# Optimization experiments

Measured on AMD Instinct MI355X. Metric: run time of the kernel, lower is better.

## Reference

```python
import jax, jax.numpy as jnp
import numpy as np

L, B, S, KV, H, D, HID, FF = 4, 16, 16, 2048, 6, 128, 768, 2048


def apply_rope(x, positions, max_wavelength=10000.0):
    # x: [B, S, H, D], positions: [B, S]; computed in float32 as in the torch code
    d_half = x.shape[-1] // 2
    freq_exponents = (2.0 / x.shape[-1]) * jnp.arange(d_half, dtype=jnp.float32)
    timescale = max_wavelength ** freq_exponents  # [d_half]
    radians = positions[..., None].astype(jnp.float32) / timescale[None, None, :]
    radians = radians[..., None, :]  # [B, S, 1, d_half]
    sin, cos = jnp.sin(radians), jnp.cos(radians)
    xf = x.astype(jnp.float32)
    x1, x2 = xf[..., :d_half], xf[..., d_half:]
    out = jnp.concatenate([x1 * cos - x2 * sin, x2 * cos + x1 * sin], axis=-1)
    return out.astype(x.dtype)


def rms_norm(x, w, eps=1e-6):
    var = jnp.mean(jnp.square(x.astype(jnp.float32)), axis=-1, keepdims=True)
    return (x.astype(jnp.float32) * jax.lax.rsqrt(var + eps)).astype(x.dtype) * w


def make_att_2d_masks(pad_masks, att_masks):
    # cumsum-comparison prefix-LM / block-causal mask (big_vision style)
    cumsum = jnp.cumsum(att_masks, axis=1)
    att_2d = cumsum[:, None, :] <= cumsum[:, :, None]
    pad_2d = pad_masks[:, None, :] & pad_masks[:, :, None]
    return att_2d & pad_2d


def setup_inputs() -> dict:
    key = jax.random.key(0)
    ks = jax.random.split(key, 20)
    sc = 0.02
    inputs_embeds = jax.random.normal(ks[0], (B, S, HID), jnp.float32)
    position_ids = jnp.broadcast_to(KV + jnp.arange(S, dtype=jnp.int64)[None, :], (B, S))
    pad_masks = jnp.ones((B, KV + S), dtype=bool)
    # prefix-LM: prefix tokens bidirectional (0), expert suffix causal (1)
    att_masks = jnp.concatenate([jnp.zeros((B, KV), jnp.int32), jnp.ones((B, S), jnp.int32)], axis=1)
    k_cache = jax.random.normal(ks[1], (L, B, H, KV, D), jnp.float32)
    v_cache = jax.random.normal(ks[2], (L, B, H, KV, D), jnp.float32)
    p = {
        'Wq': jax.random.normal(ks[3], (L, HID, H * D), jnp.float32) * sc,
        'bq': jnp.zeros((L, H * D), jnp.float32),
        'Wk': jax.random.normal(ks[4], (L, HID, H * D), jnp.float32) * sc,
        'bk': jnp.zeros((L, H * D), jnp.float32),
        'Wv': jax.random.normal(ks[5], (L, HID, H * D), jnp.float32) * sc,
        'bv': jnp.zeros((L, H * D), jnp.float32),
        'Wo': jax.random.normal(ks[6], (L, H * D, HID), jnp.float32) * sc,
        'Wg': jax.random.normal(ks[7], (L, HID, FF), jnp.float32) * sc,
        'Wu': jax.random.normal(ks[8], (L, HID, FF), jnp.float32) * sc,
        'Wd': jax.random.normal(ks[9], (L, FF, HID), jnp.float32) * sc,
        'ln1': jnp.ones((L, HID), jnp.float32),
        'ln2': jnp.ones((L, HID), jnp.float32),
        'norm_f': jnp.ones((HID,), jnp.float32),
    }
    return dict(inputs_embeds=inputs_embeds, position_ids=position_ids, pad_masks=pad_masks,
                att_masks=att_masks, k_cache=k_cache, v_cache=v_cache, **p)


def reference(inputs_embeds, position_ids, pad_masks, att_masks, k_cache, v_cache,
              Wq, bq, Wk, bk, Wv, bv, Wo, Wg, Wu, Wd, ln1, ln2, norm_f):
    b, s, _ = inputs_embeds.shape
    kv = k_cache.shape[3]
    scale = 1.0 / np.sqrt(D)
    # 2D prefix-lm mask over full prefix+suffix; expert queries are the last s rows
    mask2d = make_att_2d_masks(pad_masks, att_masks)[:, kv:, :]  # [B, S, KV+S]
    bias = jnp.where(mask2d[:, None, :, :], 0.0, -1e9).astype(inputs_embeds.dtype)
    h = inputs_embeds
    for l in range(Wq.shape[0]):
        hn = rms_norm(h, ln1[l])
        q = (hn @ Wq[l] + bq[l]).reshape(b, s, H, D)
        k = (hn @ Wk[l] + bk[l]).reshape(b, s, H, D)
        v = (hn @ Wv[l] + bv[l]).reshape(b, s, H, D)
        q = apply_rope(q, position_ids)
        k = apply_rope(k, position_ids)
        qh = jnp.swapaxes(q, 1, 2)  # [B, H, S, D]
        kf = jnp.concatenate([k_cache[l], jnp.swapaxes(k, 1, 2)], axis=2)  # [B, H, KV+S, D]
        vf = jnp.concatenate([v_cache[l], jnp.swapaxes(v, 1, 2)], axis=2)
        scores = jnp.einsum('bhqd,bhkd->bhqk', qh, kf) * scale + bias
        attn = jax.nn.softmax(scores, axis=-1)
        o = jnp.einsum('bhqk,bhkd->bhqd', attn, vf)
        o = jnp.swapaxes(o, 1, 2).reshape(b, s, H * D) @ Wo[l]
        h = h + o
        hn2 = rms_norm(h, ln2[l])
        h = h + (jax.nn.silu(hn2 @ Wg[l]) * (hn2 @ Wu[l])) @ Wd[l]
    return rms_norm(h, norm_f)
```

## Files before the change

### kernel.cpp

```cpp
#include <hip/hip_runtime.h>
#include <hip/hip_bf16.h>

#define LNUM 4
#define BB 16
#define SS 16
#define KVC 2048
#define HH 6
#define DD 128
#define HIDN 768
#define FFN 2048
#define NCH 17
#define ATT_SCALE 0.08838834764831845f
#define VT_PAD 136
#define OSH_PAD 132

typedef unsigned short u16;
typedef short s16x8 __attribute__((ext_vector_type(8)));
typedef unsigned short u16x4 __attribute__((ext_vector_type(4)));
typedef float f32x4 __attribute__((ext_vector_type(4)));

__device__ __forceinline__ short f2bfs(float f) {
    __hip_bfloat16 h = __float2bfloat16(f);
    return *reinterpret_cast<short*>(&h);
}

__global__ __launch_bounds__(64) void rope_tab_k(float2* __restrict__ tab) {
    int i = blockIdx.x * 64 + threadIdx.x;
    int s = i >> 6, d = i & 63;
    float ts = powf(10000.f, (float)d * (1.f / 64.f));
    float rad = (float)(KVC + s) / ts;
    tab[i] = make_float2(sinf(rad), cosf(rad));
}

__global__ __launch_bounds__(256) void wtrans_k(const float* __restrict__ in,
                                                u16* __restrict__ out, int K, int N) {
    int n0 = blockIdx.x * 64, k0 = blockIdx.y * 64;
    size_t moff = (size_t)blockIdx.z * K * N;
    in += moff; out += moff;
    __shared__ u16 T[64][65];
    int t = threadIdx.x;
#pragma unroll
    for (int i = 0; i < 16; ++i) {
        int idx = i * 256 + t;
        int k = idx >> 6, n = idx & 63;
        T[k][n] = (u16)f2bfs(in[(size_t)(k0 + k) * N + n0 + n]);
    }
    __syncthreads();
#pragma unroll
    for (int i = 0; i < 2; ++i) {
        int idx = i * 256 + t;
        int n = idx >> 3, kg = idx & 7;
        s16x8 v;
#pragma unroll
        for (int j = 0; j < 8; ++j) v[j] = (short)T[kg * 8 + j][n];
        *(s16x8*)(out + (size_t)(n0 + n) * K + k0 + kg * 8) = v;
    }
}

template<int OUTBF>
__global__ __launch_bounds__(64) void rmsnorm_k(const float* __restrict__ x,
                                                const float* __restrict__ w,
                                                void* __restrict__ yv) {
    int row = blockIdx.x, lane = threadIdx.x;
    const float* xp = x + (size_t)row * HIDN + lane * 12;
    float4 a = *(const float4*)xp;
    float4 b = *(const float4*)(xp + 4);
    float4 c = *(const float4*)(xp + 8);
    float s = a.x*a.x + a.y*a.y + a.z*a.z + a.w*a.w
            + b.x*b.x + b.y*b.y + b.z*b.z + b.w*b.w
            + c.x*c.x + c.y*c.y + c.z*c.z + c.w*c.w;
    for (int m = 1; m < 64; m <<= 1) s += __shfl_xor(s, m);
    float rq = rsqrtf(s * (1.f / 768.f) + 1e-6f);
    const float* wp = w + lane * 12;
    float v[12];
#pragma unroll
    for (int i = 0; i < 4; ++i) { v[i]   = (&a.x)[i] * rq * wp[i]; }
#pragma unroll
    for (int i = 0; i < 4; ++i) { v[4+i] = (&b.x)[i] * rq * wp[4+i]; }
#pragma unroll
    for (int i = 0; i < 4; ++i) { v[8+i] = (&c.x)[i] * rq * wp[8+i]; }
    if (OUTBF) {
        u16* y = (u16*)yv + (size_t)row * HIDN + lane * 12;
#pragma unroll
        for (int i = 0; i < 3; ++i) {
            u16x4 o;
#pragma unroll
            for (int j = 0; j < 4; ++j) o[j] = (u16)f2bfs(v[i * 4 + j]);
            *(u16x4*)(y + i * 4) = o;
        }
    } else {
        float* y = (float*)yv + (size_t)row * HIDN + lane * 12;
#pragma unroll
        for (int i = 0; i < 3; ++i) {
            float4 o; o.x = v[i*4]; o.y = v[i*4+1]; o.z = v[i*4+2]; o.w = v[i*4+3];
            *(float4*)(y + i * 4) = o;
        }
    }
}

__global__ __launch_bounds__(64) void qkv_k(const u16* __restrict__ hn,
                                            const u16* __restrict__ WqT, const u16* __restrict__ WkT,
                                            const u16* __restrict__ WvT,
                                            const float* __restrict__ bq, const float* __restrict__ bk,
                                            const float* __restrict__ bv,
                                            const float2* __restrict__ tab,
                                            u16* __restrict__ qr, u16* __restrict__ kr,
                                            u16* __restrict__ vr) {
    int x = blockIdx.x, b = blockIdx.y;
    int kind = x / HH, h = x % HH;
    const u16* Wt = (kind == 0) ? WqT : (kind == 1) ? WkT : WvT;
    const float* bias = (kind == 0) ? bq : (kind == 1) ? bk : bv;
    u16* outp = (kind == 0) ? qr : (kind == 1) ? kr : vr;
    int lane = threadIdx.x, r = lane & 15, qg = lane >> 4;
    f32x4 acc[8];
#pragma unroll
    for (int nt = 0; nt < 8; ++nt) acc[nt] = (f32x4){0.f, 0.f, 0.f, 0.f};
#pragma unroll 2
    for (int k0 = 0; k0 < HIDN; k0 += 32) {
        s16x8 a = *(const s16x8*)(hn + (size_t)(b * 16 + r) * HIDN + k0 + qg * 8);
#pragma unroll
        for (int nt = 0; nt < 8; ++nt) {
            s16x8 bw = *(const s16x8*)(Wt + (size_t)(h * DD + nt * 16 + r) * HIDN + k0 + qg * 8);
            acc[nt] = __builtin_amdgcn_mfma_f32_16x16x32_bf16(a, bw, acc[nt], 0, 0, 0);
        }
    }
    int bh = b * HH + h;
    if (kind < 2) {
#pragma unroll
        for (int nt = 0; nt < 4; ++nt) {
            int d1 = nt * 16 + r, d2 = d1 + 64;
            float b1 = bias[h * DD + d1], b2 = bias[h * DD + d2];
#pragma unroll
            for (int v = 0; v < 4; ++v) {
                int s = qg * 4 + v;
                float2 sc = tab[s * 64 + d1];
                float x1 = acc[nt][v] + b1;
                float x2 = acc[nt + 4][v] + b2;
                outp[(size_t)(bh * 16 + s) * DD + d1] = (u16)f2bfs(x1 * sc.y - x2 * sc.x);
                outp[(size_t)(bh * 16 + s) * DD + d2] = (u16)f2bfs(x2 * sc.y + x1 * sc.x);
            }
        }
    } else {
#pragma unroll
        for (int nt = 0; nt < 8; ++nt) {
            int d = nt * 16 + r;
            float bb = bias[h * DD + d];
#pragma unroll
            for (int v = 0; v < 4; ++v)
                outp[(size_t)(bh * 16 + qg * 4 + v) * DD + d] = (u16)f2bfs(acc[nt][v] + bb);
        }
    }
}

__global__ __launch_bounds__(256) void attn_part_k(
    const u16* __restrict__ qr, const u16* __restrict__ kr, const u16* __restrict__ vr,
    const float* __restrict__ kc, const float* __restrict__ vc,
    float* __restrict__ part_o, float* __restrict__ part_ml) {
    int bh = blockIdx.x, ch = blockIdx.y;
    int tid = threadIdx.x, wid = tid >> 6, lane = tid & 63, r = lane & 15, qg = lane >> 4;
    bool isnew = (ch == NCH - 1);
    bool active = !isnew || (wid == 0);
    __shared__ __align__(16) char smem[128 * VT_PAD * 2];
    u16* Vt = (u16*)smem;
    float* Osh = (float*)smem;
    __shared__ __align__(16) u16 Plds[4][512];
    __shared__ float mlsh[4][32];

    const float* vbase_wg = vc + ((size_t)bh * KVC + ch * 128) * DD;
    const u16* vrn = vr + (size_t)bh * SS * DD;

    if (!isnew) {
#pragma unroll
        for (int i = 0; i < 8; ++i) {
            int flat = i * 256 + tid;
            int c4 = flat & 31, rp = flat >> 5;
            const float* p0 = vbase_wg + (size_t)(2 * rp) * DD + c4 * 4;
            float4 a = *(const float4*)p0;
            float4 b = *(const float4*)(p0 + DD);
#pragma unroll
            for (int c = 0; c < 4; ++c) {
                unsigned lo = (unsigned)(u16)f2bfs((&a.x)[c]);
                unsigned hi = (unsigned)(u16)f2bfs((&b.x)[c]);
                *(unsigned*)(Vt + (size_t)(c4 * 4 + c) * VT_PAD + 2 * rp) = lo | (hi << 16);
            }
        }
    } else {
#pragma unroll
        for (int i = 0; i < 16; ++i) {
            int flat = i * 256 + tid;
            int key = flat >> 7, d = flat & 127;
            u16 v = (key < SS) ? vrn[(size_t)key * DD + d] : (u16)0;
            Vt[(size_t)d * VT_PAD + key] = v;
        }
    }
    __syncthreads();

    float mrow[4] = {-1e30f, -1e30f, -1e30f, -1e30f};
    float lrow[4] = {0.f, 0.f, 0.f, 0.f};
    f32x4 oacc[8];
#pragma unroll
    for (int nt = 0; nt < 8; ++nt) oacc[nt] = (f32x4){0.f, 0.f, 0.f, 0.f};

    if (active) {
        s16x8 aq[4];
#pragma unroll
        for (int kk = 0; kk < 4; ++kk)
            aq[kk] = *(const s16x8*)(qr + (size_t)(bh * 16 + r) * DD + kk * 32 + qg * 8);
        const float* kbase = kc + ((size_t)bh * KVC + ch * 128 + wid * 32) * DD;
        const u16* krn = kr + (size_t)bh * SS * DD;

        f32x4 st[2];
        st[0] = (f32x4){0.f,0.f,0.f,0.f};
        st[1] = (f32x4){0.f,0.f,0.f,0.f};
#pragma unroll
        for (int t = 0; t < 2; ++t) {
            if (isnew && t == 1) continue;
#pragma unroll
            for (int kk = 0; kk < 4; ++kk) {
                s16x8 bk;
                if (isnew) {
                    bk = *(const s16x8*)(krn + (size_t)(t * 16 + r) * DD + kk * 32 + qg * 8);
                } else {
                    const float* p = kbase + (size_t)(t * 16 + r) * DD + kk * 32 + qg * 8;
                    float4 xx = *(const float4*)p;
                    float4 yy = *(const float4*)(p + 4);
                    bk[0]=f2bfs(xx.x); bk[1]=f2bfs(xx.y); bk[2]=f2bfs(xx.z); bk[3]=f2bfs(xx.w);
                    bk[4]=f2bfs(yy.x); bk[5]=f2bfs(yy.y); bk[6]=f2bfs(yy.z); bk[7]=f2bfs(yy.w);
                }
                st[t] = __builtin_amdgcn_mfma_f32_16x16x32_bf16(aq[kk], bk, st[t], 0, 0, 0);
            }
        }
#pragma unroll
        for (int t = 0; t < 2; ++t)
#pragma unroll
            for (int v = 0; v < 4; ++v) st[t][v] *= ATT_SCALE;
        if (isnew) {
#pragma unroll
            for (int v = 0; v < 4; ++v) {
                if (r > qg * 4 + v) st[0][v] = -1e9f;
                st[1][v] = -1e9f;
            }
        }
#pragma unroll
        for (int v = 0; v < 4; ++v) {
            float xm = fmaxf(st[0][v], st[1][v]);
            for (int msk = 1; msk < 16; msk <<= 1) xm = fmaxf(xm, __shfl_xor(xm, msk));
            mrow[v] = xm;
        }
#pragma unroll
        for (int t = 0; t < 2; ++t)
#pragma unroll
            for (int v = 0; v < 4; ++v) st[t][v] = __expf(st[t][v] - mrow[v]);
#pragma unroll
        for (int v = 0; v < 4; ++v) {
            float ss = st[0][v] + st[1][v];
            for (int msk = 1; msk < 16; msk <<= 1) ss += __shfl_xor(ss, msk);
            lrow[v] = ss;
        }
#pragma unroll
        for (int t = 0; t < 2; ++t)
#pragma unroll
            for (int v = 0; v < 4; ++v)
                Plds[wid][(qg * 4 + v) * 32 + t * 16 + r] = (u16)f2bfs(st[t][v]);
        s16x8 ap = *(const s16x8*)(&Plds[wid][r * 32 + qg * 8]);
#pragma unroll
        for (int nt = 0; nt < 8; ++nt) {
            s16x8 bv = *(const s16x8*)(Vt + (size_t)(nt * 16 + r) * VT_PAD + wid * 32 + qg * 8);
            oacc[nt] = __builtin_amdgcn_mfma_f32_16x16x32_bf16(ap, bv, oacc[nt], 0, 0, 0);
        }
    }
    __syncthreads();
#pragma unroll
    for (int nt = 0; nt < 8; ++nt)
#pragma unroll
        for (int v = 0; v < 4; ++v)
            Osh[(size_t)(wid * 16 + qg * 4 + v) * OSH_PAD + nt * 16 + r] = oacc[nt][v];
    if (r == 0) {
#pragma unroll
        for (int v = 0; v < 4; ++v) {
            mlsh[wid][qg * 4 + v] = mrow[v];
            mlsh[wid][16 + qg * 4 + v] = lrow[v];
        }
    }
    __syncthreads();
    int q = tid >> 4, dg = tid & 15;
    float M = -1e30f;
#pragma unroll
    for (int w = 0; w < 4; ++w) M = fmaxf(M, mlsh[w][q]);
    float L = 0.f, wgt[4];
#pragma unroll
    for (int w = 0; w < 4; ++w) {
        wgt[w] = __expf(mlsh[w][q] - M);
        L += mlsh[w][16 + q] * wgt[w];
    }
    float o[8];
#pragma unroll
    for (int j = 0; j < 8; ++j) o[j] = 0.f;
#pragma unroll
    for (int w = 0; w < 4; ++w) {
        const float* op = Osh + (size_t)(w * 16 + q) * OSH_PAD + dg * 8;
        float4 a = *(const float4*)op;
        float4 b = *(const float4*)(op + 4);
        o[0]+=wgt[w]*a.x; o[1]+=wgt[w]*a.y; o[2]+=wgt[w]*a.z; o[3]+=wgt[w]*a.w;
        o[4]+=wgt[w]*b.x; o[5]+=wgt[w]*b.y; o[6]+=wgt[w]*b.z; o[7]+=wgt[w]*b.w;
    }
    float* po = part_o + ((size_t)bh * NCH + ch) * (SS * DD) + q * DD + dg * 8;
    float4 o0; o0.x=o[0]; o0.y=o[1]; o0.z=o[2]; o0.w=o[3];
    float4 o1; o1.x=o[4]; o1.y=o[5]; o1.z=o[6]; o1.w=o[7];
    *(float4*)po = o0;
    *(float4*)(po + 4) = o1;
    if (dg == 0) {
        float* pm = part_ml + ((size_t)bh * NCH + ch) * 32;
        pm[q] = M;
        pm[16 + q] = L;
    }
}

__global__ __launch_bounds__(256) void attn_comb_k(const float* __restrict__ part_o,
                                                   const float* __restrict__ part_ml,
                                                   u16* __restrict__ oa) {
    int bh = blockIdx.x, tid = threadIdx.x;
    __shared__ float sw[NCH][16], sLi[16];
    if (tid < 16) {
        float M = -1e30f;
        for (int c = 0; c < NCH; ++c) M = fmaxf(M, part_ml[((size_t)bh * NCH + c) * 32 + tid]);
        float L = 0.f;
        for (int c = 0; c < NCH; ++c) {
            const float* pm = part_ml + ((size_t)bh * NCH + c) * 32;
            float w = __expf(pm[tid] - M);
            sw[c][tid] = w;
            L += pm[16 + tid] * w;
        }
        sLi[tid] = 1.f / L;
    }
    __syncthreads();
    int q = tid >> 4, dg = tid & 15;
    float o[8];
#pragma unroll
    for (int j = 0; j < 8; ++j) o[j] = 0.f;
    for (int c = 0; c < NCH; ++c) {
        const float* po = part_o + ((size_t)bh * NCH + c) * (SS * DD) + q * DD + dg * 8;
        float4 a = *(const float4*)po;
        float4 b = *(const float4*)(po + 4);
        float w = sw[c][q];
        o[0]+=w*a.x; o[1]+=w*a.y; o[2]+=w*a.z; o[3]+=w*a.w;
        o[4]+=w*b.x; o[5]+=w*b.y; o[6]+=w*b.z; o[7]+=w*b.w;
    }
    float inv = sLi[q];
    int b = bh / HH, h = bh % HH;
    u16* yp = oa + (size_t)(b * SS + q) * HIDN + h * DD + dg * 8;
    s16x8 ov;
#pragma unroll
    for (int j = 0; j < 8; ++j) ov[j] = f2bfs(o[j] * inv);
    *(s16x8*)yp = ov;
}

template<int K, int KS>
__global__ __launch_bounds__(64) void gemm_res_k(const u16* __restrict__ A,
                                                 const u16* __restrict__ Wt,
                                                 float* __restrict__ H) {
    int lane = threadIdx.x, r = lane & 15, qg = lane >> 4;
    int n0 = blockIdx.x * 16, m0 = blockIdx.y * 16;
    const int KC = K / KS;
    int kbeg = blockIdx.z * KC;
    f32x4 acc = (f32x4){0.f, 0.f, 0.f, 0.f};
#pragma unroll 4
    for (int k0 = kbeg; k0 < kbeg + KC; k0 += 32) {
        s16x8 a  = *(const s16x8*)(A  + (size_t)(m0 + r) * K + k0 + qg * 8);
        s16x8 bw = *(const s16x8*)(Wt + (size_t)(n0 + r) * K + k0 + qg * 8);
        acc = __builtin_amdgcn_mfma_f32_16x16x32_bf16(a, bw, acc, 0, 0, 0);
    }
#pragma unroll
    for (int v = 0; v < 4; ++v) {
        size_t idx = (size_t)(m0 + qg * 4 + v) * HIDN + n0 + r;
        if (KS == 1) H[idx] += acc[v];
        else atomicAdd(&H[idx], acc[v]);
    }
}

__global__ __launch_bounds__(64) void gemm_gu_k(const u16* __restrict__ A,
                                                const u16* __restrict__ WgT,
                                                const u16* __restrict__ WuT,
                                                u16* __restrict__ F) {
    int lane = threadIdx.x, r = lane & 15, qg = lane >> 4;
    int n0 = blockIdx.x * 16, m0 = blockIdx.y * 16;
    f32x4 ag = (f32x4){0.f, 0.f, 0.f, 0.f};
    f32x4 au = (f32x4){0.f, 0.f, 0.f, 0.f};
#pragma unroll 2
    for (int k0 = 0; k0 < HIDN; k0 += 32) {
        s16x8 a  = *(const s16x8*)(A   + (size_t)(m0 + r) * HIDN + k0 + qg * 8);
        s16x8 bg = *(const s16x8*)(WgT + (size_t)(n0 + r) * HIDN + k0 + qg * 8);
        ag = __builtin_amdgcn_mfma_f32_16x16x32_bf16(a, bg, ag, 0, 0, 0);
        s16x8 bu = *(const s16x8*)(WuT + (size_t)(n0 + r) * HIDN + k0 + qg * 8);
        au = __builtin_amdgcn_mfma_f32_16x16x32_bf16(a, bu, au, 0, 0, 0);
    }
#pragma unroll
    for (int v = 0; v < 4; ++v) {
        float gv = ag[v], uv = au[v];
        float f = gv / (1.f + __expf(-gv)) * uv;
        F[(size_t)(m0 + qg * 4 + v) * FFN + n0 + r] = (u16)f2bfs(f);
    }
}

extern "C" void kernel_launch(void* const* d_in, const int* in_sizes, int n_in,
                              void* d_out, int out_size, void* d_ws, size_t ws_size,
                              hipStream_t stream) {
    (void)in_sizes; (void)n_in; (void)out_size; (void)ws_size;
    const float* emb     = (const float*)d_in[0];
    const float* k_cache = (const float*)d_in[4];
    const float* v_cache = (const float*)d_in[5];
    const float* Wq = (const float*)d_in[6];
    const float* bq = (const float*)d_in[7];
    const float* Wk = (const float*)d_in[8];
    const float* bk = (const float*)d_in[9];
    const float* Wv = (const float*)d_in[10];
    const float* bv = (const float*)d_in[11];
    const float* Wo = (const float*)d_in[12];
    const float* Wg = (const float*)d_in[13];
    const float* Wu = (const float*)d_in[14];
    const float* Wd = (const float*)d_in[15];
    const float* ln1 = (const float*)d_in[16];
    const float* ln2 = (const float*)d_in[17];
    const float* normf = (const float*)d_in[18];
    float* out = (float*)d_out;

    char* p = (char*)d_ws;
    auto alloc = [&](size_t bytes) { void* r = p; p += (bytes + 255) & ~255ull; return r; };
    const size_t WQKV = (size_t)HIDN * HH * DD;
    const size_t WMLP = (size_t)HIDN * FFN;
    u16* WqT = (u16*)alloc(LNUM * WQKV * 2);
    u16* WkT = (u16*)alloc(LNUM * WQKV * 2);
    u16* WvT = (u16*)alloc(LNUM * WQKV * 2);
    u16* WoT = (u16*)alloc(LNUM * WQKV * 2);
    u16* WgT = (u16*)alloc(LNUM * WMLP * 2);
    u16* WuT = (u16*)alloc(LNUM * WMLP * 2);
    u16* WdT = (u16*)alloc(LNUM * WMLP * 2);
    const int TOK = BB * SS;
    const size_t EMB_N = (size_t)TOK * HIDN;
    float* h  = (float*)alloc(EMB_N * 4);
    u16* hn   = (u16*)alloc(EMB_N * 2);
    u16* qr   = (u16*)alloc((size_t)BB * HH * SS * DD * 2);
    u16* kr   = (u16*)alloc((size_t)BB * HH * SS * DD * 2);
    u16* vr   = (u16*)alloc((size_t)BB * HH * SS * DD * 2);
    u16* oa   = (u16*)alloc(EMB_N * 2);
    u16* fb   = (u16*)alloc((size_t)TOK * FFN * 2);
    float* po  = (float*)alloc((size_t)96 * NCH * SS * DD * 4);
    float* pml = (float*)alloc((size_t)96 * NCH * 32 * 4);
    float2* tab = (float2*)alloc(16 * 64 * sizeof(float2));

    rope_tab_k<<<16, 64, 0, stream>>>(tab);
    wtrans_k<<<dim3(12, 12, LNUM), 256, 0, stream>>>(Wq, WqT, HIDN, HH * DD);
    wtrans_k<<<dim3(12, 12, LNUM), 256, 0, stream>>>(Wk, WkT, HIDN, HH * DD);
    wtrans_k<<<dim3(12, 12, LNUM), 256, 0, stream>>>(Wv, WvT, HIDN, HH * DD);
    wtrans_k<<<dim3(12, 12, LNUM), 256, 0, stream>>>(Wo, WoT, HH * DD, HIDN);
    wtrans_k<<<dim3(32, 12, LNUM), 256, 0, stream>>>(Wg, WgT, HIDN, FFN);
    wtrans_k<<<dim3(32, 12, LNUM), 256, 0, stream>>>(Wu, WuT, HIDN, FFN);
    wtrans_k<<<dim3(12, 32, LNUM), 256, 0, stream>>>(Wd, WdT, FFN, HIDN);

    hipMemcpyAsync(h, emb, EMB_N * sizeof(float), hipMemcpyDeviceToDevice, stream);

    const size_t KVOFF = (size_t)BB * HH * KVC * DD;
    for (int l = 0; l < LNUM; ++l) {
        rmsnorm_k<1><<<TOK, 64, 0, stream>>>(h, ln1 + l * HIDN, hn);
        qkv_k<<<dim3(3 * HH, BB), 64, 0, stream>>>(hn,
            WqT + l * WQKV, WkT + l * WQKV, WvT + l * WQKV,
            bq + l * HH * DD, bk + l * HH * DD, bv + l * HH * DD, tab, qr, kr, vr);
        attn_part_k<<<dim3(BB * HH, NCH), 256, 0, stream>>>(qr, kr, vr,
            k_cache + (size_t)l * KVOFF, v_cache + (size_t)l * KVOFF, po, pml);
        attn_comb_k<<<BB * HH, 256, 0, stream>>>(po, pml, oa);
        gemm_res_k<HH * DD, 1><<<dim3(48, 16, 1), 64, 0, stream>>>(oa, WoT + l * WQKV, h);
        rmsnorm_k<1><<<TOK, 64, 0, stream>>>(h, ln2 + l * HIDN, hn);
        gemm_gu_k<<<dim3(128, 16), 64, 0, stream>>>(hn, WgT + l * WMLP, WuT + l * WMLP, fb);
        gemm_res_k<FFN, 4><<<dim3(48, 16, 4), 64, 0, stream>>>(fb, WdT + l * WMLP, h);
    }
    rmsnorm_k<0><<<TOK, 64, 0, stream>>>(h, normf, out);
}
```

Baseline: 504.8 us.

## Fuse RMSNorm into QKV, attention combine with Wo and norm, batch transposes

Merges the seven weight-transpose launches into one kernel. RMSNorm is folded into the QKV projection, which normalises the rows into shared memory. Attention combine, the Wo projection, the residual add and the second RMSNorm become one per-batch kernel. The gate/up and down GEMMs now stage the A tile in LDS and use 256-thread blocks. This cuts launch count and global round trips for intermediates, but the combwo kernel has only 16 blocks and QKV blocks redundantly recompute the norm.

```diff
diff --git a/kernel.cpp b/kernel.cpp
--- a/kernel.cpp
+++ b/kernel.cpp
@@ -13,6 +13,9 @@
 #define ATT_SCALE 0.08838834764831845f
 #define VT_PAD 136
 #define OSH_PAD 132
+#define AP 776
+#define AP2 520
+#define HP 772
 
 typedef unsigned short u16;
 typedef short s16x8 __attribute__((ext_vector_type(8)));
@@ -32,24 +35,37 @@
     tab[i] = make_float2(sinf(rad), cosf(rad));
 }
 
-__global__ __launch_bounds__(256) void wtrans_k(const float* __restrict__ in,
-                                                u16* __restrict__ out, int K, int N) {
-    int n0 = blockIdx.x * 64, k0 = blockIdx.y * 64;
-    size_t moff = (size_t)blockIdx.z * K * N;
-    in += moff; out += moff;
+__global__ __launch_bounds__(256) void wtrans_all_k(
+    const float* __restrict__ Wq, const float* __restrict__ Wk, const float* __restrict__ Wv,
+    const float* __restrict__ Wo, const float* __restrict__ Wg, const float* __restrict__ Wu,
+    const float* __restrict__ Wd,
+    u16* __restrict__ WqT, u16* __restrict__ WkT, u16* __restrict__ WvT, u16* __restrict__ WoT,
+    u16* __restrict__ WgT, u16* __restrict__ WuT, u16* __restrict__ WdT) {
+    int idx = blockIdx.x, z = blockIdx.y;
+    const float* in; u16* out; int K, N, nx, tt;
+    if (idx < 432)      { tt = idx % 144; K = 768;  N = 768;  nx = 12;
+                          int w = idx / 144;
+                          in = (w==0)?Wq:(w==1)?Wk:Wv; out = (w==0)?WqT:(w==1)?WkT:WvT; }
+    else if (idx < 576) { tt = idx - 432; K = 768;  N = 768;  nx = 12; in = Wo; out = WoT; }
+    else if (idx < 1344){ tt = (idx - 576) % 384; K = 768; N = 2048; nx = 32;
+                          in = (idx < 960) ? Wg : Wu; out = (idx < 960) ? WgT : WuT; }
+    else                { tt = idx - 1344; K = 2048; N = 768; nx = 12; in = Wd; out = WdT; }
+    int n0 = (tt % nx) * 64, k0 = (tt / nx) * 64;
+    in  += (size_t)z * K * N;
+    out += (size_t)z * K * N;
     __shared__ u16 T[64][65];
     int t = threadIdx.x;
 #pragma unroll
     for (int i = 0; i < 16; ++i) {
-        int idx = i * 256 + t;
-        int k = idx >> 6, n = idx & 63;
+        int f = i * 256 + t;
+        int k = f >> 6, n = f & 63;
         T[k][n] = (u16)f2bfs(in[(size_t)(k0 + k) * N + n0 + n]);
     }
     __syncthreads();
 #pragma unroll
     for (int i = 0; i < 2; ++i) {
-        int idx = i * 256 + t;
-        int n = idx >> 3, kg = idx & 7;
+        int f = i * 256 + t;
+        int n = f >> 3, kg = f & 7;
         s16x8 v;
 #pragma unroll
         for (int j = 0; j < 8; ++j) v[j] = (short)T[kg * 8 + j][n];
@@ -57,10 +73,9 @@
     }
 }
 
-template<int OUTBF>
-__global__ __launch_bounds__(64) void rmsnorm_k(const float* __restrict__ x,
-                                                const float* __restrict__ w,
-                                                void* __restrict__ yv) {
+__global__ __launch_bounds__(64) void rmsnorm_f_k(const float* __restrict__ x,
+                                                  const float* __restrict__ w,
+                                                  float* __restrict__ y) {
     int row = blockIdx.x, lane = threadIdx.x;
     const float* xp = x + (size_t)row * HIDN + lane * 12;
     float4 a = *(const float4*)xp;
@@ -72,33 +87,19 @@
     for (int m = 1; m < 64; m <<= 1) s += __shfl_xor(s, m);
     float rq = rsqrtf(s * (1.f / 768.f) + 1e-6f);
     const float* wp = w + lane * 12;
-    float v[12];
-#pragma unroll
-    for (int i = 0; i < 4; ++i) { v[i]   = (&a.x)[i] * rq * wp[i]; }
-#pragma unroll
-    for (int i = 0; i < 4; ++i) { v[4+i] = (&b.x)[i] * rq * wp[4+i]; }
-#pragma unroll
-    for (int i = 0; i < 4; ++i) { v[8+i] = (&c.x)[i] * rq * wp[8+i]; }
-    if (OUTBF) {
-        u16* y = (u16*)yv + (size_t)row * HIDN + lane * 12;
-#pragma unroll
-        for (int i = 0; i < 3; ++i) {
-            u16x4 o;
-#pragma unroll
-            for (int j = 0; j < 4; ++j) o[j] = (u16)f2bfs(v[i * 4 + j]);
-            *(u16x4*)(y + i * 4) = o;
-        }
-    } else {
-        float* y = (float*)yv + (size_t)row * HIDN + lane * 12;
-#pragma unroll
-        for (int i = 0; i < 3; ++i) {
-            float4 o; o.x = v[i*4]; o.y = v[i*4+1]; o.z = v[i*4+2]; o.w = v[i*4+3];
-            *(float4*)(y + i * 4) = o;
-        }
-    }
-}
-
-__global__ __launch_bounds__(64) void qkv_k(const u16* __restrict__ hn,
+    float* yp = y + (size_t)row * HIDN + lane * 12;
+#pragma unroll
+    for (int i = 0; i < 3; ++i) {
+        float4 xv = (i == 0) ? a : (i == 1) ? b : c;
+        float4 o;
+        o.x = xv.x*rq*wp[i*4]; o.y = xv.y*rq*wp[i*4+1];
+        o.z = xv.z*rq*wp[i*4+2]; o.w = xv.w*rq*wp[i*4+3];
+        *(float4*)(yp + i * 4) = o;
+    }
+}
+
+__global__ __launch_bounds__(64) void qkv_k(const float* __restrict__ h,
+                                            const float* __restrict__ ln1w,
                                             const u16* __restrict__ WqT, const u16* __restrict__ WkT,
                                             const u16* __restrict__ WvT,
                                             const float* __restrict__ bq, const float* __restrict__ bk,
@@ -107,29 +108,52 @@
                                             u16* __restrict__ qr, u16* __restrict__ kr,
                                             u16* __restrict__ vr) {
     int x = blockIdx.x, b = blockIdx.y;
-    int kind = x / HH, h = x % HH;
+    int kind = x / HH, hh = x % HH;
     const u16* Wt = (kind == 0) ? WqT : (kind == 1) ? WkT : WvT;
     const float* bias = (kind == 0) ? bq : (kind == 1) ? bk : bv;
     u16* outp = (kind == 0) ? qr : (kind == 1) ? kr : vr;
     int lane = threadIdx.x, r = lane & 15, qg = lane >> 4;
+    __shared__ u16 A[16][AP];
+    float wln[12];
+#pragma unroll
+    for (int i = 0; i < 12; ++i) wln[i] = ln1w[lane * 12 + i];
+    for (int row = 0; row < 16; ++row) {
+        const float* xp = h + (size_t)(b * 16 + row) * HIDN + lane * 12;
+        float4 a = *(const float4*)xp;
+        float4 bb = *(const float4*)(xp + 4);
+        float4 c = *(const float4*)(xp + 8);
+        float s = a.x*a.x + a.y*a.y + a.z*a.z + a.w*a.w
+                + bb.x*bb.x + bb.y*bb.y + bb.z*bb.z + bb.w*bb.w
+                + c.x*c.x + c.y*c.y + c.z*c.z + c.w*c.w;
+        for (int m = 1; m < 64; m <<= 1) s += __shfl_xor(s, m);
+        float rq = rsqrtf(s * (1.f / 768.f) + 1e-6f);
+        u16x4 o;
+#pragma unroll
+        for (int i = 0; i < 3; ++i) {
+            float4 xv = (i == 0) ? a : (i == 1) ? bb : c;
+#pragma unroll
+            for (int j = 0; j < 4; ++j) o[j] = (u16)f2bfs((&xv.x)[j] * rq * wln[i*4+j]);
+            *(u16x4*)(&A[row][lane * 12 + i * 4]) = o;
+        }
+    }
     f32x4 acc[8];
 #pragma unroll
     for (int nt = 0; nt < 8; ++nt) acc[nt] = (f32x4){0.f, 0.f, 0.f, 0.f};
 #pragma unroll 2
     for (int k0 = 0; k0 < HIDN; k0 += 32) {
-        s16x8 a = *(const s16x8*)(hn + (size_t)(b * 16 + r) * HIDN + k0 + qg * 8);
+        s16x8 a = *(const s16x8*)(&A[r][k0 + qg * 8]);
 #pragma unroll
         for (int nt = 0; nt < 8; ++nt) {
-            s16x8 bw = *(const s16x8*)(Wt + (size_t)(h * DD + nt * 16 + r) * HIDN + k0 + qg * 8);
+            s16x8 bw = *(const s16x8*)(Wt + (size_t)(hh * DD + nt * 16 + r) * HIDN + k0 + qg * 8);
             acc[nt] = __builtin_amdgcn_mfma_f32_16x16x32_bf16(a, bw, acc[nt], 0, 0, 0);
         }
     }
-    int bh = b * HH + h;
+    int bh = b * HH + hh;
     if (kind < 2) {
 #pragma unroll
         for (int nt = 0; nt < 4; ++nt) {
             int d1 = nt * 16 + r, d2 = d1 + 64;
-            float b1 = bias[h * DD + d1], b2 = bias[h * DD + d2];
+            float b1 = bias[hh * DD + d1], b2 = bias[hh * DD + d2];
 #pragma unroll
             for (int v = 0; v < 4; ++v) {
                 int s = qg * 4 + v;
@@ -144,7 +168,7 @@
 #pragma unroll
         for (int nt = 0; nt < 8; ++nt) {
             int d = nt * 16 + r;
-            float bb = bias[h * DD + d];
+            float bb = bias[hh * DD + d];
 #pragma unroll
             for (int v = 0; v < 4; ++v)
                 outp[(size_t)(bh * 16 + qg * 4 + v) * DD + d] = (u16)f2bfs(acc[nt][v] + bb);
@@ -316,79 +340,103 @@
     }
 }
 
-__global__ __launch_bounds__(256) void attn_comb_k(const float* __restrict__ part_o,
-                                                   const float* __restrict__ part_ml,
-                                                   u16* __restrict__ oa) {
-    int bh = blockIdx.x, tid = threadIdx.x;
-    __shared__ float sw[NCH][16], sLi[16];
-    if (tid < 16) {
+__global__ __launch_bounds__(512) void combwo_k(const float* __restrict__ part_o,
+                                                const float* __restrict__ part_ml,
+                                                const u16* __restrict__ WoT,
+                                                const float* __restrict__ ln2w,
+                                                float* __restrict__ h,
+                                                u16* __restrict__ hn) {
+    int b = blockIdx.x, tid = threadIdx.x;
+    __shared__ u16 oaL[16][AP];
+    __shared__ float hnewL[16][HP];
+    int q = tid >> 5, dg = tid & 31;
+#pragma unroll
+    for (int hh = 0; hh < HH; ++hh) {
+        int bh = b * HH + hh;
+        const float* pm = part_ml + (size_t)bh * NCH * 32;
         float M = -1e30f;
-        for (int c = 0; c < NCH; ++c) M = fmaxf(M, part_ml[((size_t)bh * NCH + c) * 32 + tid]);
+#pragma unroll
+        for (int c = 0; c < NCH; ++c) M = fmaxf(M, pm[c * 32 + q]);
         float L = 0.f;
+        float o[4] = {0.f, 0.f, 0.f, 0.f};
+#pragma unroll
         for (int c = 0; c < NCH; ++c) {
-            const float* pm = part_ml + ((size_t)bh * NCH + c) * 32;
-            float w = __expf(pm[tid] - M);
-            sw[c][tid] = w;
-            L += pm[16 + tid] * w;
-        }
-        sLi[tid] = 1.f / L;
-    }
-    __syncthreads();
-    int q = tid >> 4, dg = tid & 15;
-    float o[8];
-#pragma unroll
-    for (int j = 0; j < 8; ++j) o[j] = 0.f;
-    for (int c = 0; c < NCH; ++c) {
-        const float* po = part_o + ((size_t)bh * NCH + c) * (SS * DD) + q * DD + dg * 8;
-        float4 a = *(const float4*)po;
-        float4 b = *(const float4*)(po + 4);
-        float w = sw[c][q];
-        o[0]+=w*a.x; o[1]+=w*a.y; o[2]+=w*a.z; o[3]+=w*a.w;
-        o[4]+=w*b.x; o[5]+=w*b.y; o[6]+=w*b.z; o[7]+=w*b.w;
-    }
-    float inv = sLi[q];
-    int b = bh / HH, h = bh % HH;
-    u16* yp = oa + (size_t)(b * SS + q) * HIDN + h * DD + dg * 8;
-    s16x8 ov;
-#pragma unroll
-    for (int j = 0; j < 8; ++j) ov[j] = f2bfs(o[j] * inv);
-    *(s16x8*)yp = ov;
-}
-
-template<int K, int KS>
-__global__ __launch_bounds__(64) void gemm_res_k(const u16* __restrict__ A,
-                                                 const u16* __restrict__ Wt,
-                                                 float* __restrict__ H) {
-    int lane = threadIdx.x, r = lane & 15, qg = lane >> 4;
-    int n0 = blockIdx.x * 16, m0 = blockIdx.y * 16;
-    const int KC = K / KS;
-    int kbeg = blockIdx.z * KC;
-    f32x4 acc = (f32x4){0.f, 0.f, 0.f, 0.f};
-#pragma unroll 4
-    for (int k0 = kbeg; k0 < kbeg + KC; k0 += 32) {
-        s16x8 a  = *(const s16x8*)(A  + (size_t)(m0 + r) * K + k0 + qg * 8);
-        s16x8 bw = *(const s16x8*)(Wt + (size_t)(n0 + r) * K + k0 + qg * 8);
-        acc = __builtin_amdgcn_mfma_f32_16x16x32_bf16(a, bw, acc, 0, 0, 0);
-    }
-#pragma unroll
-    for (int v = 0; v < 4; ++v) {
-        size_t idx = (size_t)(m0 + qg * 4 + v) * HIDN + n0 + r;
-        if (KS == 1) H[idx] += acc[v];
-        else atomicAdd(&H[idx], acc[v]);
-    }
-}
-
-__global__ __launch_bounds__(64) void gemm_gu_k(const u16* __restrict__ A,
-                                                const u16* __restrict__ WgT,
-                                                const u16* __restrict__ WuT,
-                                                u16* __restrict__ F) {
-    int lane = threadIdx.x, r = lane & 15, qg = lane >> 4;
-    int n0 = blockIdx.x * 16, m0 = blockIdx.y * 16;
+            float w = __expf(pm[c * 32 + q] - M);
+            L += pm[c * 32 + 16 + q] * w;
+            const float* po = part_o + ((size_t)bh * NCH + c) * (SS * DD) + q * DD + dg * 4;
+            float4 pv = *(const float4*)po;
+            o[0] += w * pv.x; o[1] += w * pv.y; o[2] += w * pv.z; o[3] += w * pv.w;
+        }
+        float inv = 1.f / L;
+        u16x4 ov;
+#pragma unroll
+        for (int j = 0; j < 4; ++j) ov[j] = (u16)f2bfs(o[j] * inv);
+        *(u16x4*)(&oaL[q][hh * DD + dg * 4]) = ov;
+    }
+    __syncthreads();
+    int wid = tid >> 6, lane = tid & 63, r = lane & 15, qg = lane >> 4;
+    f32x4 acc[6];
+#pragma unroll
+    for (int nt = 0; nt < 6; ++nt) acc[nt] = (f32x4){0.f, 0.f, 0.f, 0.f};
+#pragma unroll 2
+    for (int k0 = 0; k0 < HIDN; k0 += 32) {
+        s16x8 a = *(const s16x8*)(&oaL[r][k0 + qg * 8]);
+#pragma unroll
+        for (int nt = 0; nt < 6; ++nt) {
+            s16x8 bw = *(const s16x8*)(WoT + (size_t)(wid * 96 + nt * 16 + r) * HIDN + k0 + qg * 8);
+            acc[nt] = __builtin_amdgcn_mfma_f32_16x16x32_bf16(a, bw, acc[nt], 0, 0, 0);
+        }
+    }
+#pragma unroll
+    for (int nt = 0; nt < 6; ++nt)
+#pragma unroll
+        for (int v = 0; v < 4; ++v) {
+            int row = qg * 4 + v, col = wid * 96 + nt * 16 + r;
+            size_t idx = (size_t)(b * 16 + row) * HIDN + col;
+            float hv = h[idx] + acc[nt][v];
+            h[idx] = hv;
+            hnewL[row][col] = hv;
+        }
+    __syncthreads();
+    int row = tid >> 5, c0 = (tid & 31) * 24;
+    float s = 0.f;
+#pragma unroll
+    for (int i = 0; i < 24; ++i) { float x = hnewL[row][c0 + i]; s += x * x; }
+#pragma unroll
+    for (int m = 1; m < 32; m <<= 1) s += __shfl_xor(s, m);
+    float rq = rsqrtf(s * (1.f / 768.f) + 1e-6f);
+    u16* yp = hn + (size_t)(b * 16 + row) * HIDN + c0;
+#pragma unroll
+    for (int i = 0; i < 6; ++i) {
+        u16x4 o;
+#pragma unroll
+        for (int j = 0; j < 4; ++j)
+            o[j] = (u16)f2bfs(hnewL[row][c0 + i * 4 + j] * rq * ln2w[c0 + i * 4 + j]);
+        *(u16x4*)(yp + i * 4) = o;
+    }
+}
+
+__global__ __launch_bounds__(256) void gemm_gu_k(const u16* __restrict__ hn,
+                                                 const u16* __restrict__ WgT,
+                                                 const u16* __restrict__ WuT,
+                                                 u16* __restrict__ F) {
+    int tid = threadIdx.x, wid = tid >> 6, lane = tid & 63, r = lane & 15, qg = lane >> 4;
+    int m0 = blockIdx.y * 16;
+    __shared__ u16 A[16][AP];
+#pragma unroll
+    for (int i = 0; i < 6; ++i) {
+        int idx8 = i * 256 + tid;
+        int row = idx8 / 96, c8 = idx8 % 96;
+        s16x8 v = *(const s16x8*)(hn + (size_t)(m0 + row) * HIDN + c8 * 8);
+        *(s16x8*)(&A[row][c8 * 8]) = v;
+    }
+    __syncthreads();
+    int n0 = blockIdx.x * 64 + wid * 16;
     f32x4 ag = (f32x4){0.f, 0.f, 0.f, 0.f};
     f32x4 au = (f32x4){0.f, 0.f, 0.f, 0.f};
 #pragma unroll 2
     for (int k0 = 0; k0 < HIDN; k0 += 32) {
-        s16x8 a  = *(const s16x8*)(A   + (size_t)(m0 + r) * HIDN + k0 + qg * 8);
+        s16x8 a  = *(const s16x8*)(&A[r][k0 + qg * 8]);
         s16x8 bg = *(const s16x8*)(WgT + (size_t)(n0 + r) * HIDN + k0 + qg * 8);
         ag = __builtin_amdgcn_mfma_f32_16x16x32_bf16(a, bg, ag, 0, 0, 0);
         s16x8 bu = *(const s16x8*)(WuT + (size_t)(n0 + r) * HIDN + k0 + qg * 8);
@@ -400,6 +448,34 @@
         float f = gv / (1.f + __expf(-gv)) * uv;
         F[(size_t)(m0 + qg * 4 + v) * FFN + n0 + r] = (u16)f2bfs(f);
     }
+}
+
+__global__ __launch_bounds__(256) void gemm_down_k(const u16* __restrict__ F,
+                                                   const u16* __restrict__ WdT,
+                                                   float* __restrict__ H) {
+    int tid = threadIdx.x, wid = tid >> 6, lane = tid & 63, r = lane & 15, qg = lane >> 4;
+    int m0 = blockIdx.y * 16;
+    int kbeg = blockIdx.z * 512;
+    __shared__ u16 A[16][AP2];
+#pragma unroll
+    for (int i = 0; i < 4; ++i) {
+        int idx8 = i * 256 + tid;
+        int row = idx8 / 64, c8 = idx8 % 64;
+        s16x8 v = *(const s16x8*)(F + (size_t)(m0 + row) * FFN + kbeg + c8 * 8);
+        *(s16x8*)(&A[row][c8 * 8]) = v;
+    }
+    __syncthreads();
+    int n0 = blockIdx.x * 64 + wid * 16;
+    f32x4 acc = (f32x4){0.f, 0.f, 0.f, 0.f};
+#pragma unroll 4
+    for (int k0 = 0; k0 < 512; k0 += 32) {
+        s16x8 a  = *(const s16x8*)(&A[r][k0 + qg * 8]);
+        s16x8 bw = *(const s16x8*)(WdT + (size_t)(n0 + r) * FFN + kbeg + k0 + qg * 8);
+        acc = __builtin_amdgcn_mfma_f32_16x16x32_bf16(a, bw, acc, 0, 0, 0);
+    }
+#pragma unroll
+    for (int v = 0; v < 4; ++v)
+        atomicAdd(&H[(size_t)(m0 + qg * 4 + v) * HIDN + n0 + r], acc[v]);
 }
 
 extern "C" void kernel_launch(void* const* d_in, const int* in_sizes, int n_in,
@@ -442,36 +518,26 @@
     u16* qr   = (u16*)alloc((size_t)BB * HH * SS * DD * 2);
     u16* kr   = (u16*)alloc((size_t)BB * HH * SS * DD * 2);
     u16* vr   = (u16*)alloc((size_t)BB * HH * SS * DD * 2);
-    u16* oa   = (u16*)alloc(EMB_N * 2);
     u16* fb   = (u16*)alloc((size_t)TOK * FFN * 2);
     float* po  = (float*)alloc((size_t)96 * NCH * SS * DD * 4);
     float* pml = (float*)alloc((size_t)96 * NCH * 32 * 4);
     float2* tab = (float2*)alloc(16 * 64 * sizeof(float2));
 
     rope_tab_k<<<16, 64, 0, stream>>>(tab);
-    wtrans_k<<<dim3(12, 12, LNUM), 256, 0, stream>>>(Wq, WqT, HIDN, HH * DD);
-    wtrans_k<<<dim3(12, 12, LNUM), 256, 0, stream>>>(Wk, WkT, HIDN, HH * DD);
-    wtrans_k<<<dim3(12, 12, LNUM), 256, 0, stream>>>(Wv, WvT, HIDN, HH * DD);
-    wtrans_k<<<dim3(12, 12, LNUM), 256, 0, stream>>>(Wo, WoT, HH * DD, HIDN);
-    wtrans_k<<<dim3(32, 12, LNUM), 256, 0, stream>>>(Wg, WgT, HIDN, FFN);
-    wtrans_k<<<dim3(32, 12, LNUM), 256, 0, stream>>>(Wu, WuT, HIDN, FFN);
-    wtrans_k<<<dim3(12, 32, LNUM), 256, 0, stream>>>(Wd, WdT, FFN, HIDN);
-
+    wtrans_all_k<<<dim3(1728, LNUM), 256, 0, stream>>>(Wq, Wk, Wv, Wo, Wg, Wu, Wd,
+                                                       WqT, WkT, WvT, WoT, WgT, WuT, WdT);
     hipMemcpyAsync(h, emb, EMB_N * sizeof(float), hipMemcpyDeviceToDevice, stream);
 
     const size_t KVOFF = (size_t)BB * HH * KVC * DD;
     for (int l = 0; l < LNUM; ++l) {
-        rmsnorm_k<1><<<TOK, 64, 0, stream>>>(h, ln1 + l * HIDN, hn);
-        qkv_k<<<dim3(3 * HH, BB), 64, 0, stream>>>(hn,
+        qkv_k<<<dim3(3 * HH, BB), 64, 0, stream>>>(h, ln1 + l * HIDN,
             WqT + l * WQKV, WkT + l * WQKV, WvT + l * WQKV,
             bq + l * HH * DD, bk + l * HH * DD, bv + l * HH * DD, tab, qr, kr, vr);
         attn_part_k<<<dim3(BB * HH, NCH), 256, 0, stream>>>(qr, kr, vr,
             k_cache + (size_t)l * KVOFF, v_cache + (size_t)l * KVOFF, po, pml);
-        attn_comb_k<<<BB * HH, 256, 0, stream>>>(po, pml, oa);
-        gemm_res_k<HH * DD, 1><<<dim3(48, 16, 1), 64, 0, stream>>>(oa, WoT + l * WQKV, h);
-        rmsnorm_k<1><<<TOK, 64, 0, stream>>>(h, ln2 + l * HIDN, hn);
-        gemm_gu_k<<<dim3(128, 16), 64, 0, stream>>>(hn, WgT + l * WMLP, WuT + l * WMLP, fb);
-        gemm_res_k<FFN, 4><<<dim3(48, 16, 4), 64, 0, stream>>>(fb, WdT + l * WMLP, h);
-    }
-    rmsnorm_k<0><<<TOK, 64, 0, stream>>>(h, normf, out);
-}
+        combwo_k<<<BB, 512, 0, stream>>>(po, pml, WoT + l * WQKV, ln2 + l * HIDN, h, hn);
+        gemm_gu_k<<<dim3(32, 16), 256, 0, stream>>>(hn, WgT + l * WMLP, WuT + l * WMLP, fb);
+        gemm_down_k<<<dim3(12, 16, 4), 256, 0, stream>>>(fb, WdT + l * WMLP, h);
+    }
+    rmsnorm_f_k<<<TOK, 64, 0, stream>>>(h, normf, out);
+}
```

Measured after the change: 610.8 us. 21.0% more time.
